# Optimization experiments

Hardware: AMD Instinct MI355X
Metric: run time of the kernel (lower is better)

Reference implementation:

```python
import jax, jax.numpy as jnp
import numpy as np

S, I, H, O = 4096, 64, 1024, 1


def setup_inputs() -> dict:
    key = jax.random.key(0)
    ks = jax.random.split(key, 8)
    k = 1.0 / np.sqrt(H)  # torch LSTM/Linear init scale
    u = lambda kk, shp: jax.random.uniform(kk, shp, jnp.float32, -k, k)
    return {
        "input_seq": jax.random.normal(ks[0], (S, I), jnp.float32),
        "W_ih": u(ks[1], (4 * H, I)),
        "W_hh": u(ks[2], (4 * H, H)),
        "b_ih": u(ks[3], (4 * H,)),
        "b_hh": u(ks[4], (4 * H,)),
        "W_lin": u(ks[5], (O, H)),
        "b_lin": u(ks[6], (O,)),
    }


def reference(input_seq, W_ih, W_hh, b_ih, b_hh, W_lin, b_lin):
    # Precompute input contributions to all gates in one GEMM: [S, 4H]
    x_gates = input_seq @ W_ih.T + (b_ih + b_hh)

    def step(carry, xg):
        h, c = carry
        g = xg + h @ W_hh.T  # [4H], gate order i, f, g, o (torch convention)
        i, f, gg, o = jnp.split(g, 4)
        i = jax.nn.sigmoid(i)
        f = jax.nn.sigmoid(f)
        gg = jnp.tanh(gg)
        o = jax.nn.sigmoid(o)
        c = f * c + i * gg
        h = o * jnp.tanh(c)
        return (h, c), None

    h0 = jnp.zeros((H,), x_gates.dtype)
    c0 = jnp.zeros((H,), x_gates.dtype)
    (h_last, _), _ = jax.lax.scan(step, (h0, c0), x_gates)
    # original applies linear to every step then takes [-1]; equivalent to
    # projecting only the last hidden state
    return h_last @ W_lin.T + b_lin  # [O]
```

## Files before the change

kernel.cpp:

```cpp
#include <hip/hip_runtime.h>


#define SEQ_LEN 4096
#define HID 1024
#define NBLK 128
#define TPB 512
#define HPB 8

#define ALD(p)    __hip_atomic_load((p), __ATOMIC_RELAXED, __HIP_MEMORY_SCOPE_AGENT)
#define AST(p,v)  __hip_atomic_store((p), (v), __ATOMIC_RELAXED, __HIP_MEMORY_SCOPE_AGENT)

__device__ __forceinline__ float fast_sigmoid(float x) {
    return __builtin_amdgcn_rcpf(1.0f + __builtin_amdgcn_exp2f(-1.4426950408889634f * x));
}
__device__ __forceinline__ float fast_tanh(float x) {
    return fmaf(-2.0f, __builtin_amdgcn_rcpf(1.0f + __builtin_amdgcn_exp2f(2.8853900817779268f * x)), 1.0f);
}

__global__ void lstm_init_kernel(unsigned long long* ws) {
    int t = threadIdx.x;
    #pragma unroll
    for (int k = 0; k < 8; ++k) ws[t + 256 * k] = 0ull;
}

__global__ __launch_bounds__(TPB, 1) void lstm_persistent_kernel(
    const float* __restrict__ input,
    const float* __restrict__ W_ih,
    const float* __restrict__ W_hh,
    const float* __restrict__ b_ih,
    const float* __restrict__ b_hh,
    const float* __restrict__ W_lin,
    const float* __restrict__ b_lin,
    float* __restrict__ out,
    unsigned long long* __restrict__ ws)
{
    const int t   = threadIdx.x;
    const int b   = blockIdx.x;
    const int w   = t >> 6;
    const int l   = t & 63;
    const int grp = l >> 4;
    const int sl  = l & 15;
    const int j   = HPB * b + w;
    const int row = grp * HID + j;

    unsigned long long* slot0 = ws;
    unsigned long long* slot1 = ws + HID;

    __shared__ float4 wlds4[17 * TPB];
    __shared__ float  hs[2][HID];
    __shared__ unsigned long long pub[HPB];
    __shared__ float  red[HPB];

    {
        const float4* Whh4 = (const float4*)(W_hh + (size_t)row * HID);
        #pragma unroll
        for (int c = 0; c < 16; ++c)
            wlds4[c * TPB + t] = Whh4[sl + 16 * c];
        wlds4[16 * TPB + t] = ((const float4*)(W_ih + (size_t)row * 64))[sl];
    }
    float bias[4];
    #pragma unroll
    for (int q = 0; q < 4; ++q) bias[q] = b_ih[q * HID + j] + b_hh[q * HID + j];
    if (t < HPB) pub[t] = 0ull;
    __syncthreads();

    const float4 W0  = wlds4[ 0 * TPB + t];
    const float4 W1  = wlds4[ 1 * TPB + t];
    const float4 W2  = wlds4[ 2 * TPB + t];
    const float4 W3  = wlds4[ 3 * TPB + t];
    const float4 W4  = wlds4[ 4 * TPB + t];
    const float4 W5  = wlds4[ 5 * TPB + t];
    const float4 W6  = wlds4[ 6 * TPB + t];
    const float4 W7  = wlds4[ 7 * TPB + t];
    const float4 W8  = wlds4[ 8 * TPB + t];
    const float4 W9  = wlds4[ 9 * TPB + t];
    const float4 W10 = wlds4[10 * TPB + t];
    const float4 W11 = wlds4[11 * TPB + t];
    const float4 W12 = wlds4[12 * TPB + t];
    const float4 W13 = wlds4[13 * TPB + t];
    const float4 W14 = wlds4[14 * TPB + t];
    const float4 W15 = wlds4[15 * TPB + t];
    const float4 W16 = wlds4[16 * TPB + t];

    const float4* xin4 = (const float4*)input;
    float c_state = 0.0f;

    for (int s = 0; s < SEQ_LEN; ++s) {
        float4 x4 = xin4[s * 16 + sl];

        unsigned long long* rs = (s & 1) ? slot1 : slot0;
        const unsigned tag = (unsigned)s;
        unsigned long long v0, v1;
        {
            unsigned long long a0 = ALD(&rs[t]), a1 = ALD(&rs[t + 512]);
            for (;;) {
                unsigned long long b0 = ALD(&rs[t]), b1 = ALD(&rs[t + 512]);
                if (((unsigned)(a0 >> 32) == tag) & ((unsigned)(a1 >> 32) == tag)) {
                    v0 = a0; v1 = a1; break;
                }
                a0 = ALD(&rs[t]); a1 = ALD(&rs[t + 512]);
                if (((unsigned)(b0 >> 32) == tag) & ((unsigned)(b1 >> 32) == tag)) {
                    v0 = b0; v1 = b1; break;
                }
            }
        }

        float* hsb = hs[s & 1];
        hsb[t      ] = __uint_as_float((unsigned)(v0 & 0xffffffffull));
        hsb[t + 512] = __uint_as_float((unsigned)(v1 & 0xffffffffull));

        __syncthreads();

        const float4* hs4 = (const float4*)hsb;
        float a0 = 0.f, a1 = 0.f, a2 = 0.f, a3 = 0.f;
        #define FMA_CHUNK(Wc, c, acc) { float4 h4_ = hs4[16 * (c) + sl];      \
            acc = fmaf((Wc).x, h4_.x, acc); acc = fmaf((Wc).y, h4_.y, acc);   \
            acc = fmaf((Wc).z, h4_.z, acc); acc = fmaf((Wc).w, h4_.w, acc); }
        FMA_CHUNK(W0,  0, a0) FMA_CHUNK(W1,  1, a1)
        FMA_CHUNK(W2,  2, a2) FMA_CHUNK(W3,  3, a3)
        FMA_CHUNK(W4,  4, a0) FMA_CHUNK(W5,  5, a1)
        FMA_CHUNK(W6,  6, a2) FMA_CHUNK(W7,  7, a3)
        FMA_CHUNK(W8,  8, a0) FMA_CHUNK(W9,  9, a1)
        FMA_CHUNK(W10, 10, a2) FMA_CHUNK(W11, 11, a3)
        FMA_CHUNK(W12, 12, a0) FMA_CHUNK(W13, 13, a1)
        FMA_CHUNK(W14, 14, a2) FMA_CHUNK(W15, 15, a3)
        #undef FMA_CHUNK
        a0 = fmaf(W16.x, x4.x, a0); a1 = fmaf(W16.y, x4.y, a1);
        a2 = fmaf(W16.z, x4.z, a2); a3 = fmaf(W16.w, x4.w, a3);
        float acc = (a0 + a1) + (a2 + a3);

        acc += __shfl_xor(acc, 1);
        acc += __shfl_xor(acc, 2);
        acc += __shfl_xor(acc, 4);
        acc += __shfl_xor(acc, 8);

        float gi = __shfl(acc, 0)  + bias[0];
        float gf = __shfl(acc, 16) + bias[1];
        float gg = __shfl(acc, 32) + bias[2];
        float go = __shfl(acc, 48) + bias[3];

        float ig = fast_sigmoid(gi);
        float fg = fast_sigmoid(gf);
        float cg = fast_tanh(gg);
        float og = fast_sigmoid(go);
        c_state  = fmaf(fg, c_state, ig * cg);
        float hn = og * fast_tanh(c_state);

        const unsigned ntag = (unsigned)(s + 1);
        if (l == 0) {
            unsigned long long pv = ((unsigned long long)ntag << 32) |
                                    (unsigned long long)__float_as_uint(hn);
            __hip_atomic_store(&pub[w], pv, __ATOMIC_RELAXED, __HIP_MEMORY_SCOPE_WORKGROUP);
        }
        if (w == 0 && l < HPB) {
            unsigned long long pv;
            do {
                pv = __hip_atomic_load(&pub[l], __ATOMIC_RELAXED, __HIP_MEMORY_SCOPE_WORKGROUP);
            } while ((unsigned)(pv >> 32) != ntag);
            unsigned long long* wsl = (s & 1) ? slot0 : slot1;
            AST(&wsl[HPB * b + l], pv);
        }
    }

    if (b == 0) {
        const unsigned tag = (unsigned)SEQ_LEN;
        unsigned long long v0, v1;
        bool r0 = false, r1 = false;
        do {
            if (!r0) { v0 = ALD(&slot0[t      ]); r0 = ((unsigned)(v0 >> 32) == tag); }
            if (!r1) { v1 = ALD(&slot0[t + 512]); r1 = ((unsigned)(v1 >> 32) == tag); }
        } while (!(r0 && r1));
        float p = __uint_as_float((unsigned)(v0 & 0xffffffffull)) * W_lin[t] +
                  __uint_as_float((unsigned)(v1 & 0xffffffffull)) * W_lin[t + 512];
        #pragma unroll
        for (int m = 32; m >= 1; m >>= 1) p += __shfl_xor(p, m);
        if (l == 0) red[w] = p;
        __syncthreads();
        if (t == 0) {
            float r = 0.f;
            #pragma unroll
            for (int k = 0; k < HPB; ++k) r += red[k];
            out[0] = r + b_lin[0];
        }
    }
}

extern "C" void kernel_launch(void* const* d_in, const int* in_sizes, int n_in,
                              void* d_out, int out_size, void* d_ws, size_t ws_size,
                              hipStream_t stream) {
    const float* input = (const float*)d_in[0];
    const float* W_ih  = (const float*)d_in[1];
    const float* W_hh  = (const float*)d_in[2];
    const float* b_ih  = (const float*)d_in[3];
    const float* b_hh  = (const float*)d_in[4];
    const float* W_lin = (const float*)d_in[5];
    const float* b_lin = (const float*)d_in[6];
    float* out = (float*)d_out;
    unsigned long long* ws = (unsigned long long*)d_ws;

    hipLaunchKernelGGL(lstm_init_kernel, dim3(1), dim3(256), 0, stream, ws);

    void* args[] = { (void*)&input, (void*)&W_ih, (void*)&W_hh, (void*)&b_ih,
                     (void*)&b_hh, (void*)&W_lin, (void*)&b_lin, (void*)&out, (void*)&ws };
    (void)hipLaunchCooperativeKernel((void*)lstm_persistent_kernel, dim3(NBLK), dim3(TPB),
                                     args, 0, stream);
}
```

Baseline: 9.112 ms.

## Replace per-step block barrier with per-chunk LDS flags for hidden-state readiness

Each wave now writes its slice of the gathered hidden state into LDS and raises a per-chunk flag instead of everyone waiting at a workgroup barrier. Consumers spin on each chunk's flag just before using it, so the dot product can begin on chunks that are already ready while others are still arriving. The input-projection term is moved to the start of the accumulation, and the global poll loop is simplified so each half latches once it sees the right tag. In exchange, many waves spin on LDS flags, and correctness rests on signal fences and relaxed workgroup-scope atomics ordering the plain LDS stores, which is fragile.

```diff
diff --git a/kernel.cpp b/kernel.cpp
--- a/kernel.cpp
+++ b/kernel.cpp
@@ -9,6 +9,8 @@
 
 #define ALD(p)    __hip_atomic_load((p), __ATOMIC_RELAXED, __HIP_MEMORY_SCOPE_AGENT)
 #define AST(p,v)  __hip_atomic_store((p), (v), __ATOMIC_RELAXED, __HIP_MEMORY_SCOPE_AGENT)
+#define LLDU(p)   __hip_atomic_load((p), __ATOMIC_RELAXED, __HIP_MEMORY_SCOPE_WORKGROUP)
+#define LSTU(p,v) __hip_atomic_store((p), (v), __ATOMIC_RELAXED, __HIP_MEMORY_SCOPE_WORKGROUP)
 
 __device__ __forceinline__ float fast_sigmoid(float x) {
     return __builtin_amdgcn_rcpf(1.0f + __builtin_amdgcn_exp2f(-1.4426950408889634f * x));
@@ -48,6 +50,7 @@
 
     __shared__ float4 wlds4[17 * TPB];
     __shared__ float  hs[2][HID];
+    __shared__ unsigned fl[2][16];
     __shared__ unsigned long long pub[HPB];
     __shared__ float  red[HPB];
 
@@ -62,6 +65,7 @@
     #pragma unroll
     for (int q = 0; q < 4; ++q) bias[q] = b_ih[q * HID + j] + b_hh[q * HID + j];
     if (t < HPB) pub[t] = 0ull;
+    if (t < 32) ((unsigned*)fl)[t] = 0xFFFFFFFFu;
     __syncthreads();
 
     const float4 W0  = wlds4[ 0 * TPB + t];
@@ -86,35 +90,36 @@
     float c_state = 0.0f;
 
     for (int s = 0; s < SEQ_LEN; ++s) {
+        const int par = s & 1;
         float4 x4 = xin4[s * 16 + sl];
 
-        unsigned long long* rs = (s & 1) ? slot1 : slot0;
+        unsigned long long* rs = par ? slot1 : slot0;
         const unsigned tag = (unsigned)s;
         unsigned long long v0, v1;
-        {
-            unsigned long long a0 = ALD(&rs[t]), a1 = ALD(&rs[t + 512]);
-            for (;;) {
-                unsigned long long b0 = ALD(&rs[t]), b1 = ALD(&rs[t + 512]);
-                if (((unsigned)(a0 >> 32) == tag) & ((unsigned)(a1 >> 32) == tag)) {
-                    v0 = a0; v1 = a1; break;
-                }
-                a0 = ALD(&rs[t]); a1 = ALD(&rs[t + 512]);
-                if (((unsigned)(b0 >> 32) == tag) & ((unsigned)(b1 >> 32) == tag)) {
-                    v0 = b0; v1 = b1; break;
-                }
-            }
-        }
-
-        float* hsb = hs[s & 1];
+        bool q0 = false, q1 = false;
+        do {
+            if (!q0) { v0 = ALD(&rs[t      ]); q0 = ((unsigned)(v0 >> 32) == tag); }
+            if (!q1) { v1 = ALD(&rs[t + 512]); q1 = ((unsigned)(v1 >> 32) == tag); }
+        } while (!(q0 && q1));
+
+        float* hsb = hs[par];
         hsb[t      ] = __uint_as_float((unsigned)(v0 & 0xffffffffull));
         hsb[t + 512] = __uint_as_float((unsigned)(v1 & 0xffffffffull));
-
-        __syncthreads();
+        __atomic_signal_fence(__ATOMIC_RELEASE);
+        if (l == 0) {
+            LSTU(&fl[par][w],     tag);
+            LSTU(&fl[par][w + 8], tag);
+        }
 
         const float4* hs4 = (const float4*)hsb;
-        float a0 = 0.f, a1 = 0.f, a2 = 0.f, a3 = 0.f;
-        #define FMA_CHUNK(Wc, c, acc) { float4 h4_ = hs4[16 * (c) + sl];      \
-            acc = fmaf((Wc).x, h4_.x, acc); acc = fmaf((Wc).y, h4_.y, acc);   \
+        volatile unsigned* flp = &fl[par][0];
+        float a0 = W16.x * x4.x, a1 = W16.y * x4.y,
+              a2 = W16.z * x4.z, a3 = W16.w * x4.w;
+        #define FMA_CHUNK(Wc, c, acc) {                                        \
+            while (LLDU((unsigned*)&flp[(c)]) != tag) { }                      \
+            __atomic_signal_fence(__ATOMIC_ACQUIRE);                           \
+            float4 h4_ = hs4[16 * (c) + sl];                                   \
+            acc = fmaf((Wc).x, h4_.x, acc); acc = fmaf((Wc).y, h4_.y, acc);    \
             acc = fmaf((Wc).z, h4_.z, acc); acc = fmaf((Wc).w, h4_.w, acc); }
         FMA_CHUNK(W0,  0, a0) FMA_CHUNK(W1,  1, a1)
         FMA_CHUNK(W2,  2, a2) FMA_CHUNK(W3,  3, a3)
@@ -125,8 +130,6 @@
         FMA_CHUNK(W12, 12, a0) FMA_CHUNK(W13, 13, a1)
         FMA_CHUNK(W14, 14, a2) FMA_CHUNK(W15, 15, a3)
         #undef FMA_CHUNK
-        a0 = fmaf(W16.x, x4.x, a0); a1 = fmaf(W16.y, x4.y, a1);
-        a2 = fmaf(W16.z, x4.z, a2); a3 = fmaf(W16.w, x4.w, a3);
         float acc = (a0 + a1) + (a2 + a3);
 
         acc += __shfl_xor(acc, 1);
@@ -157,7 +160,7 @@
             do {
                 pv = __hip_atomic_load(&pub[l], __ATOMIC_RELAXED, __HIP_MEMORY_SCOPE_WORKGROUP);
             } while ((unsigned)(pv >> 32) != ntag);
-            unsigned long long* wsl = (s & 1) ? slot0 : slot1;
+            unsigned long long* wsl = par ? slot0 : slot1;
             AST(&wsl[HPB * b + l], pv);
         }
     }
@@ -165,11 +168,11 @@
     if (b == 0) {
         const unsigned tag = (unsigned)SEQ_LEN;
         unsigned long long v0, v1;
-        bool r0 = false, r1 = false;
+        bool q0 = false, q1 = false;
         do {
-            if (!r0) { v0 = ALD(&slot0[t      ]); r0 = ((unsigned)(v0 >> 32) == tag); }
-            if (!r1) { v1 = ALD(&slot0[t + 512]); r1 = ((unsigned)(v1 >> 32) == tag); }
-        } while (!(r0 && r1));
+            if (!q0) { v0 = ALD(&slot0[t      ]); q0 = ((unsigned)(v0 >> 32) == tag); }
+            if (!q1) { v1 = ALD(&slot0[t + 512]); q1 = ((unsigned)(v1 >> 32) == tag); }
+        } while (!(q0 && q1));
         float p = __uint_as_float((unsigned)(v0 & 0xffffffffull)) * W_lin[t] +
                   __uint_as_float((unsigned)(v1 & 0xffffffffull)) * W_lin[t + 512];
         #pragma unroll
```

Result: slower. 10.01 ms (+9.9%).

## Replace per-element tagged h exchange with per-block flags and separate data buffer

Applied to the files above, without the earlier changes.

Instead of every thread spinning on 64-bit tag+value words for all 1024 hidden elements, the kernel now stores h values as plain 32-bit data and publishes one release-ordered tag per block. Only wave 0 polls the 128 block flags, then a barrier lets all threads read the data. This cuts polling traffic and the width of exchanged words. The trade-off is an extra __syncthreads per step and reliance on relaxed data loads being ordered by the flag's release store, with no acquire on the reader side.

```diff
diff --git a/kernel.cpp b/kernel.cpp
--- a/kernel.cpp
+++ b/kernel.cpp
@@ -7,8 +7,8 @@
 #define TPB 512
 #define HPB 8
 
-#define ALD(p)    __hip_atomic_load((p), __ATOMIC_RELAXED, __HIP_MEMORY_SCOPE_AGENT)
-#define AST(p,v)  __hip_atomic_store((p), (v), __ATOMIC_RELAXED, __HIP_MEMORY_SCOPE_AGENT)
+#define ALD4(p)   __hip_atomic_load((p), __ATOMIC_RELAXED, __HIP_MEMORY_SCOPE_AGENT)
+#define AST4(p,v) __hip_atomic_store((p), (v), __ATOMIC_RELAXED, __HIP_MEMORY_SCOPE_AGENT)
 
 __device__ __forceinline__ float fast_sigmoid(float x) {
     return __builtin_amdgcn_rcpf(1.0f + __builtin_amdgcn_exp2f(-1.4426950408889634f * x));
@@ -43,8 +43,8 @@
     const int j   = HPB * b + w;
     const int row = grp * HID + j;
 
-    unsigned long long* slot0 = ws;
-    unsigned long long* slot1 = ws + HID;
+    unsigned* dat = (unsigned*)ws;
+    unsigned* tg  = (unsigned*)(ws + 1024);
 
     __shared__ float4 wlds4[17 * TPB];
     __shared__ float  hs[2][HID];
@@ -86,28 +86,27 @@
     float c_state = 0.0f;
 
     for (int s = 0; s < SEQ_LEN; ++s) {
+        const int par = s & 1;
         float4 x4 = xin4[s * 16 + sl];
 
-        unsigned long long* rs = (s & 1) ? slot1 : slot0;
-        const unsigned tag = (unsigned)s;
-        unsigned long long v0, v1;
-        {
-            unsigned long long a0 = ALD(&rs[t]), a1 = ALD(&rs[t + 512]);
-            for (;;) {
-                unsigned long long b0 = ALD(&rs[t]), b1 = ALD(&rs[t + 512]);
-                if (((unsigned)(a0 >> 32) == tag) & ((unsigned)(a1 >> 32) == tag)) {
-                    v0 = a0; v1 = a1; break;
-                }
-                a0 = ALD(&rs[t]); a1 = ALD(&rs[t + 512]);
-                if (((unsigned)(b0 >> 32) == tag) & ((unsigned)(b1 >> 32) == tag)) {
-                    v0 = b0; v1 = b1; break;
-                }
-            }
-        }
-
-        float* hsb = hs[s & 1];
-        hsb[t      ] = __uint_as_float((unsigned)(v0 & 0xffffffffull));
-        hsb[t + 512] = __uint_as_float((unsigned)(v1 & 0xffffffffull));
+        if (w == 0) {
+            unsigned* tp = tg + (par << 7);
+            const unsigned tag = (unsigned)s;
+            unsigned u0, u1;
+            bool q0 = false, q1 = false;
+            do {
+                if (!q0) { u0 = ALD4(&tp[l]);      q0 = (u0 == tag); }
+                if (!q1) { u1 = ALD4(&tp[l + 64]); q1 = (u1 == tag); }
+            } while (!(q0 && q1));
+        }
+        __syncthreads();
+
+        unsigned* dp = dat + (par << 10);
+        unsigned u0 = ALD4(&dp[t]);
+        unsigned u1 = ALD4(&dp[t + 512]);
+        float* hsb = hs[par];
+        hsb[t      ] = __uint_as_float(u0);
+        hsb[t + 512] = __uint_as_float(u1);
 
         __syncthreads();
 
@@ -152,26 +151,37 @@
                                     (unsigned long long)__float_as_uint(hn);
             __hip_atomic_store(&pub[w], pv, __ATOMIC_RELAXED, __HIP_MEMORY_SCOPE_WORKGROUP);
         }
-        if (w == 0 && l < HPB) {
-            unsigned long long pv;
+        if (w == 0) {
+            const int npar = (s + 1) & 1;
+            if (l < HPB) {
+                unsigned long long pv;
+                do {
+                    pv = __hip_atomic_load(&pub[l], __ATOMIC_RELAXED, __HIP_MEMORY_SCOPE_WORKGROUP);
+                } while ((unsigned)(pv >> 32) != ntag);
+                AST4(&dat[(npar << 10) + HPB * b + l], (unsigned)(pv & 0xffffffffull));
+            }
+            if (l == 0) {
+                __hip_atomic_store(&tg[(npar << 7) + b], ntag,
+                                   __ATOMIC_RELEASE, __HIP_MEMORY_SCOPE_AGENT);
+            }
+        }
+    }
+
+    if (b == 0) {
+        if (w == 0) {
+            const unsigned tag = (unsigned)SEQ_LEN;
+            unsigned u0, u1;
+            bool q0 = false, q1 = false;
             do {
-                pv = __hip_atomic_load(&pub[l], __ATOMIC_RELAXED, __HIP_MEMORY_SCOPE_WORKGROUP);
-            } while ((unsigned)(pv >> 32) != ntag);
-            unsigned long long* wsl = (s & 1) ? slot0 : slot1;
-            AST(&wsl[HPB * b + l], pv);
-        }
-    }
-
-    if (b == 0) {
-        const unsigned tag = (unsigned)SEQ_LEN;
-        unsigned long long v0, v1;
-        bool r0 = false, r1 = false;
-        do {
-            if (!r0) { v0 = ALD(&slot0[t      ]); r0 = ((unsigned)(v0 >> 32) == tag); }
-            if (!r1) { v1 = ALD(&slot0[t + 512]); r1 = ((unsigned)(v1 >> 32) == tag); }
-        } while (!(r0 && r1));
-        float p = __uint_as_float((unsigned)(v0 & 0xffffffffull)) * W_lin[t] +
-                  __uint_as_float((unsigned)(v1 & 0xffffffffull)) * W_lin[t + 512];
+                if (!q0) { u0 = ALD4(&tg[l]);      q0 = (u0 == tag); }
+                if (!q1) { u1 = ALD4(&tg[l + 64]); q1 = (u1 == tag); }
+            } while (!(q0 && q1));
+        }
+        __syncthreads();
+        unsigned u0 = ALD4(&dat[t]);
+        unsigned u1 = ALD4(&dat[t + 512]);
+        float p = __uint_as_float(u0) * W_lin[t] +
+                  __uint_as_float(u1) * W_lin[t + 512];
         #pragma unroll
         for (int m = 32; m >= 1; m >>= 1) p += __shfl_xor(p, m);
         if (l == 0) red[w] = p;
```

Result: slower. 21.77 ms (+139.0%).
